# Performance work log

Hardware: AMD Instinct MI355X
Metric: run time of the kernel (lower is better)

The kernel has to match this reference:

```python
import jax, jax.numpy as jnp
import numpy as np

BLOCK = 8
ITERS = 8
EPS = 1e-5
SHAPE = (64, 64, 64)
BATCH = 16


def overlapping_blocks(x, bs):
    # x: [B, M, N, K] -> per-block copies with a 1-cell zero-padded halo:
    # [B, nm, nn, nk, bs+2, bs+2, bs+2]
    B, M, N, K = x.shape
    p = jnp.pad(x, ((0, 0), (1, 1), (1, 1), (1, 1)))

    def gather(a, axis, n, size):
        idx = (jnp.arange(n)[:, None] * bs + jnp.arange(size)[None, :]).reshape(-1)
        a = jnp.take(a, idx, axis=axis)
        return a.reshape(a.shape[:axis] + (n, size) + a.shape[axis + 1:])

    nm, nn, nk = M // bs, N // bs, K // bs
    p = gather(p, 1, nm, bs + 2)   # [B, nm, P, N+2, K+2]
    p = gather(p, 3, nn, bs + 2)   # [B, nm, P, nn, P, K+2]
    p = gather(p, 5, nk, bs + 2)   # [B, nm, P, nn, P, nk, P]
    return p.transpose(0, 1, 3, 5, 2, 4, 6)


def param_blocks(w, bs):
    # [..., M, N, K] -> [..., nm, nn, nk, bs, bs, bs] (non-overlapping)
    lead = w.shape[:-3]
    M, N, K = w.shape[-3:]
    w = w.reshape(*lead, M // bs, bs, N // bs, bs, K // bs, bs)
    nl = len(lead)
    perm = tuple(range(nl)) + (nl, nl + 2, nl + 4, nl + 1, nl + 3, nl + 5)
    return w.transpose(perm)


def gridnet_step(weight, bias, residual_scale, x, inner_iterations, block_size,
                 eps=EPS, normalize=True):
    bs = block_size
    blocks = overlapping_blocks(x, bs)            # [B, nm, nn, nk, P, P, P]
    wb = param_blocks(weight, bs)                 # [27, nm, nn, nk, bs, bs, bs]
    bb = param_blocks(bias, bs)                   # [nm, nn, nk, bs, bs, bs]
    rb = param_blocks(residual_scale, bs)
    inner = (slice(None),) * 4 + (slice(1, -1),) * 3

    for _ in range(inner_iterations):
        if normalize:
            mean = blocks.mean(axis=(-3, -2, -1), keepdims=True)
            var = blocks.var(axis=(-3, -2, -1), keepdims=True)
            normed = (blocks - mean) / jnp.sqrt(var + eps)
        else:
            normed = blocks
        dot = jnp.zeros_like(blocks[inner])
        tap = 0
        for dx in range(3):
            for dy in range(3):
                for dz in range(3):
                    nb = normed[..., dx:dx + bs, dy:dy + bs, dz:dz + bs]
                    dot = dot + nb * wb[tap]
                    tap += 1
        out = blocks[inner] + rb * jax.nn.silu(dot + bb)
        # only interior cells update; halo stays at initial (synced) values
        blocks = blocks.at[inner].set(out)

    y = blocks[inner]                              # [B, nm, nn, nk, bs, bs, bs]
    B, nm, nn, nk = y.shape[:4]
    return y.transpose(0, 1, 4, 2, 5, 3, 6).reshape(B, nm * bs, nn * bs, nk * bs)


def setup_inputs() -> dict:
    key = jax.random.key(0)
    k_w, k_x = jax.random.split(key)
    M, N, K = SHAPE
    weight = jax.random.normal(k_w, (27, M, N, K), dtype=jnp.float32) / np.sqrt(27.0).astype(np.float32)
    bias = jnp.zeros((M, N, K), dtype=jnp.float32)
    residual_scale = jnp.ones((M, N, K), dtype=jnp.float32)
    x = jax.random.normal(k_x, (BATCH, M, N, K), dtype=jnp.float32)
    return {"weight": weight, "bias": bias, "residual_scale": residual_scale, "x": x}


def reference(weight, bias, residual_scale, x):
    return gridnet_step(weight, bias, residual_scale, x, ITERS, BLOCK, EPS, True)
```

## Files before the change

kernel.cpp:

```cpp
#include <hip/hip_runtime.h>

typedef _Float16 h2 __attribute__((ext_vector_type(2)));

#define CSTR 7
#define COLH 14

template <int CTRL>
__device__ __forceinline__ float dpp_stage(float v) {
    int x = __builtin_amdgcn_update_dpp(0, __float_as_int(v), CTRL, 0xf, 0xf, true);
    return v + __int_as_float(x);
}
__device__ __forceinline__ float wave_sum(float v) {
    v = dpp_stage<0x111>(v);
    v = dpp_stage<0x112>(v);
    v = dpp_stage<0x114>(v);
    v = dpp_stage<0x118>(v);
    v = dpp_stage<0x142>(v);
    v = dpp_stage<0x143>(v);
    return v;
}

#define RFL(x) __int_as_float(__builtin_amdgcn_readfirstlane(__float_as_int(x)))

__device__ __forceinline__ h2 mid2(h2 lo, h2 hi) {
    int r = __builtin_amdgcn_alignbit(__builtin_bit_cast(int, hi),
                                      __builtin_bit_cast(int, lo), 16);
    return __builtin_bit_cast(h2, r);
}
__device__ __forceinline__ h2 pkrtz(float a, float b) {
    return __builtin_bit_cast(h2, __builtin_amdgcn_cvt_pkrtz(a, b));
}

#define R27(M) M(0) M(1) M(2) M(3) M(4) M(5) M(6) M(7) M(8) M(9) M(10) M(11) \
    M(12) M(13) M(14) M(15) M(16) M(17) M(18) M(19) M(20) M(21) M(22) M(23)  \
    M(24) M(25) M(26)

#define LOADW(T)                                                               \
    float4 f##T = *(const float4*)(W + ((size_t)(T) << 18) + ofs);             \
    h2 w##T##p = pkrtz(f##T.x, f##T.y);                                        \
    h2 w##T##q = pkrtz(f##T.z, f##T.w);                                        \
    sw0 += f##T.x; sw1 += f##T.y; sw2 += f##T.z; sw3 += f##T.w;

#define COLN(BP, O, T0, T1, T2) {                                              \
    h2 d0 = BP[(O)], d1 = BP[(O) + 1], d2 = BP[(O) + 2];                       \
    h2 m0 = mid2(d0, d1), m1 = mid2(d1, d2);                                   \
    dd0 = __builtin_elementwise_fma(d0, w##T0##p, dd0);                        \
    dd1 = __builtin_elementwise_fma(d1, w##T0##q, dd1);                        \
    dd0 = __builtin_elementwise_fma(m0, w##T1##p, dd0);                        \
    dd1 = __builtin_elementwise_fma(m1, w##T1##q, dd1);                        \
    dd0 = __builtin_elementwise_fma(d1, w##T2##p, dd0);                        \
    dd1 = __builtin_elementwise_fma(d2, w##T2##q, dd1); }

#define SILU(U) ((U) * __builtin_amdgcn_rcpf(1.f + __expf(-(U))))

#define ITERX(BP, DSTB, RED) {                                                 \
    h2 dd0 = { (_Float16)0.f, (_Float16)0.f };                                 \
    h2 dd1 = dd0;                                                              \
    COLN(BP, 0,    0,  1,  2)                                                  \
    COLN(BP, 7,    3,  4,  5)                                                  \
    COLN(BP, 14,   6,  7,  8)                                                  \
    COLN(BP, 70,   9, 10, 11)                                                  \
    COLN(BP, 77,  12, 13, 14)                                                  \
    COLN(BP, 84,  15, 16, 17)                                                  \
    COLN(BP, 140, 18, 19, 20)                                                  \
    COLN(BP, 147, 21, 22, 23)                                                  \
    COLN(BP, 154, 24, 25, 26)                                                  \
    float mean = (halo_s + Si) * inv_n;                                        \
    float istd = rsqrtf((halo_q + Qi) * inv_n - mean * mean + 1e-5f);          \
    float u0 = ((float)dd0.x - mean * sw0) * istd + bf.x;                      \
    float u1 = ((float)dd0.y - mean * sw1) * istd + bf.y;                      \
    float u2 = ((float)dd1.x - mean * sw2) * istd + bf.z;                      \
    float u3 = ((float)dd1.y - mean * sw3) * istd + bf.w;                      \
    c0 += rf.x * SILU(u0);                                                     \
    c1 += rf.y * SILU(u1);                                                     \
    c2 += rf.z * SILU(u2);                                                     \
    c3 += rf.w * SILU(u3);                                                     \
    DSTB[ipc] = (_Float16)c0;                                                  \
    *(h2*)&DSTB[ipc + 1] = pkrtz(c1, c2);                                      \
    DSTB[ipc + 3] = (_Float16)c3;                                              \
    float sp = wave_sum((c0 + c1) + (c2 + c3));                                \
    float qp = wave_sum((c0 * c0 + c1 * c1) + (c2 * c2 + c3 * c3));            \
    if (lane == 63) RED[bh][wv1] = make_float2(sp, qp);                        \
    __syncthreads();                                                           \
    Si = RFL(RED[bh][0].x + RED[bh][1].x);                                     \
    Qi = RFL(RED[bh][0].y + RED[bh][1].y); }

__global__ __launch_bounds__(256)
void gridnet_kernel(const float* __restrict__ W,
                    const float* __restrict__ Bias,
                    const float* __restrict__ Rs,
                    const float* __restrict__ X,
                    float* __restrict__ Y,
                    int n_batch)
{
    __shared__ __align__(16) _Float16 bufA0[100 * COLH];
    __shared__ __align__(16) _Float16 bufA1[100 * COLH];
    __shared__ __align__(16) _Float16 bufB0[100 * COLH];
    __shared__ __align__(16) _Float16 bufB1[100 * COLH];
    __shared__ float4 red4[2][4];
    __shared__ float2 redP[2][2][2];

    const int tid = threadIdx.x;
    const int h    = tid & 1;
    const int ly   = (tid >> 1) & 7;
    const int lx   = (tid >> 4) & 7;
    const int bh   = tid >> 7;
    const int wave = tid >> 6;
    const int lane = tid & 63;
    const int wv1  = wave & 1;

    const int np    = n_batch >> 1;
    const int bid   = blockIdx.x;
    const int r     = bid / np;
    const int pb    = bid - r * np;
    const int batch2 = 2 * pb;
    const int gm0 = (r >> 6) << 3;
    const int gn0 = ((r >> 3) & 7) << 3;
    const int gk0 = (r & 7) << 3;

    const float* xb = X + ((size_t)batch2 << 18);

    float sA_all = 0.f, qA_all = 0.f, sA_int = 0.f, qA_int = 0.f;
    float sB_all = 0.f, qB_all = 0.f, sB_int = 0.f, qB_int = 0.f;
    for (int i = tid; i < 1000; i += 256) {
        int ix = i / 100;
        int rem = i - ix * 100;
        int iy = rem / 10;
        int iz = rem - iy * 10;
        int m = gm0 + ix - 1, n = gn0 + iy - 1, k = gk0 + iz - 1;
        float vA = 0.f, vB = 0.f;
        if ((unsigned)m < 64u && (unsigned)n < 64u && (unsigned)k < 64u) {
            const float* p = xb + (m << 12) + (n << 6) + k;
            vA = p[0];
            vB = p[1 << 18];
        }
        _Float16 hA = (_Float16)vA, hB = (_Float16)vB;
        int a = (ix * 10 + iy) * COLH + iz;
        bufA0[a] = hA; bufA1[a] = hA;
        bufB0[a] = hB; bufB1[a] = hB;
        float fA = (float)hA, fB = (float)hB;
        sA_all += fA; qA_all += fA * fA;
        sB_all += fB; qB_all += fB * fB;
        bool interior = ((unsigned)(ix - 1) < 8u) & ((unsigned)(iy - 1) < 8u) &
                        ((unsigned)(iz - 1) < 8u);
        if (interior) { sA_int += fA; qA_int += fA * fA;
                        sB_int += fB; qB_int += fB * fB; }
    }

    const int gm = gm0 + lx, gn = gn0 + ly;
    const size_t ofs = ((size_t)gm << 12) + (gn << 6) + gk0 + 4 * h;
    float sw0 = 0.f, sw1 = 0.f, sw2 = 0.f, sw3 = 0.f;
    R27(LOADW)
    const float4 bf = *(const float4*)(Bias + ofs);
    const float4 rf = *(const float4*)(Rs + ofs);

    {
        float a0 = wave_sum(sA_all), a1 = wave_sum(qA_all);
        float a2 = wave_sum(sA_int), a3 = wave_sum(qA_int);
        float b0 = wave_sum(sB_all), b1 = wave_sum(qB_all);
        float b2 = wave_sum(sB_int), b3 = wave_sum(qB_int);
        if (lane == 63) {
            red4[0][wave] = make_float4(a0, a1, a2, a3);
            red4[1][wave] = make_float4(b0, b1, b2, b3);
        }
    }
    __syncthreads();

    float S_all = 0.f, Q_all = 0.f, Si = 0.f, Qi = 0.f;
    #pragma unroll
    for (int wv = 0; wv < 4; ++wv) {
        float4 t = red4[bh][wv];
        S_all += t.x; Q_all += t.y; Si += t.z; Qi += t.w;
    }
    const float halo_s = RFL(S_all - Si);
    const float halo_q = RFL(Q_all - Qi);
    Si = RFL(Si); Qi = RFL(Qi);

    _Float16* const my0 = bh ? bufB0 : bufA0;
    _Float16* const my1 = bh ? bufB1 : bufA1;
    const int bpD = (lx * 10 + ly) * CSTR + 2 * h;
    const h2* const bp0 = (const h2*)my0 + bpD;
    const h2* const bp1 = (const h2*)my1 + bpD;
    const int ipc = ((lx + 1) * 10 + (ly + 1)) * COLH + 4 * h + 1;
    float c0 = (float)my0[ipc],     c1 = (float)my0[ipc + 1];
    float c2 = (float)my0[ipc + 2], c3 = (float)my0[ipc + 3];

    const float inv_n = 1.0f / 1000.0f;

    #pragma unroll 1
    for (int it = 0; it < 4; ++it) {
        ITERX(bp0, my1, redP[0])
        ITERX(bp1, my0, redP[1])
    }

    float* yp = Y + ((size_t)(batch2 + bh) << 18) + ofs;
    *(float4*)yp = make_float4(c0, c1, c2, c3);
}

extern "C" void kernel_launch(void* const* d_in, const int* in_sizes, int n_in,
                              void* d_out, int out_size, void* d_ws, size_t ws_size,
                              hipStream_t stream) {
    const float* W = (const float*)d_in[0];
    const float* B = (const float*)d_in[1];
    const float* R = (const float*)d_in[2];
    const float* X = (const float*)d_in[3];
    float* Y = (float*)d_out;

    int n_batch = in_sizes[3] >> 18;
    dim3 grid(512 * (n_batch >> 1)), block(256);
    hipLaunchKernelGGL(gridnet_kernel, grid, block, 0, stream, W, B, R, X, Y, n_batch);
}
```

Before: 167.7 us.

## Process four batch samples per block, two per thread, sharing weight registers

Each block now handles four batch samples instead of two, and each 128-thread half computes two samples per thread. The 27 packed weight taps, bias and residual scale loaded per thread are reused across both samples. This halves the grid size and the weight loads per sample, and merges two samples' reductions into a single barrier per iteration. The cost is doubled LDS usage, more live registers (two sets of accumulators and stats), and fewer blocks to hide latency.

```diff
diff --git a/kernel.cpp b/kernel.cpp
--- a/kernel.cpp
+++ b/kernel.cpp
@@ -41,49 +41,62 @@
     h2 w##T##q = pkrtz(f##T.z, f##T.w);                                        \
     sw0 += f##T.x; sw1 += f##T.y; sw2 += f##T.z; sw3 += f##T.w;
 
-#define COLN(BP, O, T0, T1, T2) {                                              \
+#define COLN(BP, O, T0, T1, T2, D0N, D1N) {                                    \
     h2 d0 = BP[(O)], d1 = BP[(O) + 1], d2 = BP[(O) + 2];                       \
     h2 m0 = mid2(d0, d1), m1 = mid2(d1, d2);                                   \
-    dd0 = __builtin_elementwise_fma(d0, w##T0##p, dd0);                        \
-    dd1 = __builtin_elementwise_fma(d1, w##T0##q, dd1);                        \
-    dd0 = __builtin_elementwise_fma(m0, w##T1##p, dd0);                        \
-    dd1 = __builtin_elementwise_fma(m1, w##T1##q, dd1);                        \
-    dd0 = __builtin_elementwise_fma(d1, w##T2##p, dd0);                        \
-    dd1 = __builtin_elementwise_fma(d2, w##T2##q, dd1); }
+    D0N = __builtin_elementwise_fma(d0, w##T0##p, D0N);                        \
+    D1N = __builtin_elementwise_fma(d1, w##T0##q, D1N);                        \
+    D0N = __builtin_elementwise_fma(m0, w##T1##p, D0N);                        \
+    D1N = __builtin_elementwise_fma(m1, w##T1##q, D1N);                        \
+    D0N = __builtin_elementwise_fma(d1, w##T2##p, D0N);                        \
+    D1N = __builtin_elementwise_fma(d2, w##T2##q, D1N); }
+
+#define DOT27(BP, D0N, D1N)                                                    \
+    COLN(BP, 0,    0,  1,  2, D0N, D1N)                                        \
+    COLN(BP, 7,    3,  4,  5, D0N, D1N)                                        \
+    COLN(BP, 14,   6,  7,  8, D0N, D1N)                                        \
+    COLN(BP, 70,   9, 10, 11, D0N, D1N)                                        \
+    COLN(BP, 77,  12, 13, 14, D0N, D1N)                                        \
+    COLN(BP, 84,  15, 16, 17, D0N, D1N)                                        \
+    COLN(BP, 140, 18, 19, 20, D0N, D1N)                                        \
+    COLN(BP, 147, 21, 22, 23, D0N, D1N)                                        \
+    COLN(BP, 154, 24, 25, 26, D0N, D1N)
 
 #define SILU(U) ((U) * __builtin_amdgcn_rcpf(1.f + __expf(-(U))))
 
-#define ITERX(BP, DSTB, RED) {                                                 \
-    h2 dd0 = { (_Float16)0.f, (_Float16)0.f };                                 \
-    h2 dd1 = dd0;                                                              \
-    COLN(BP, 0,    0,  1,  2)                                                  \
-    COLN(BP, 7,    3,  4,  5)                                                  \
-    COLN(BP, 14,   6,  7,  8)                                                  \
-    COLN(BP, 70,   9, 10, 11)                                                  \
-    COLN(BP, 77,  12, 13, 14)                                                  \
-    COLN(BP, 84,  15, 16, 17)                                                  \
-    COLN(BP, 140, 18, 19, 20)                                                  \
-    COLN(BP, 147, 21, 22, 23)                                                  \
-    COLN(BP, 154, 24, 25, 26)                                                  \
-    float mean = (halo_s + Si) * inv_n;                                        \
-    float istd = rsqrtf((halo_q + Qi) * inv_n - mean * mean + 1e-5f);          \
-    float u0 = ((float)dd0.x - mean * sw0) * istd + bf.x;                      \
-    float u1 = ((float)dd0.y - mean * sw1) * istd + bf.y;                      \
-    float u2 = ((float)dd1.x - mean * sw2) * istd + bf.z;                      \
-    float u3 = ((float)dd1.y - mean * sw3) * istd + bf.w;                      \
-    c0 += rf.x * SILU(u0);                                                     \
-    c1 += rf.y * SILU(u1);                                                     \
-    c2 += rf.z * SILU(u2);                                                     \
-    c3 += rf.w * SILU(u3);                                                     \
-    DSTB[ipc] = (_Float16)c0;                                                  \
-    *(h2*)&DSTB[ipc + 1] = pkrtz(c1, c2);                                      \
-    DSTB[ipc + 3] = (_Float16)c3;                                              \
-    float sp = wave_sum((c0 + c1) + (c2 + c3));                                \
-    float qp = wave_sum((c0 * c0 + c1 * c1) + (c2 * c2 + c3 * c3));            \
-    if (lane == 63) RED[bh][wv1] = make_float2(sp, qp);                        \
+#define EPI4(DD0, DD1, SI, QI, HS, HQ, C0, C1, C2, C3, DSTB) {                 \
+    float mean = (HS + SI) * inv_n;                                            \
+    float istd = rsqrtf((HQ + QI) * inv_n - mean * mean + 1e-5f);              \
+    float u0 = ((float)DD0.x - mean * sw0) * istd + bf.x;                      \
+    float u1 = ((float)DD0.y - mean * sw1) * istd + bf.y;                      \
+    float u2 = ((float)DD1.x - mean * sw2) * istd + bf.z;                      \
+    float u3 = ((float)DD1.y - mean * sw3) * istd + bf.w;                      \
+    C0 += rf.x * SILU(u0);                                                     \
+    C1 += rf.y * SILU(u1);                                                     \
+    C2 += rf.z * SILU(u2);                                                     \
+    C3 += rf.w * SILU(u3);                                                     \
+    DSTB[ipc] = (_Float16)C0;                                                  \
+    *(h2*)&DSTB[ipc + 1] = pkrtz(C1, C2);                                      \
+    DSTB[ipc + 3] = (_Float16)C3;  }
+
+#define ITERP(BPA, DSTA, BPB, DSTB, RED) {                                     \
+    h2 ddA0 = { (_Float16)0.f, (_Float16)0.f };                                \
+    h2 ddA1 = ddA0, ddB0 = ddA0, ddB1 = ddA0;                                  \
+    DOT27(BPA, ddA0, ddA1)                                                     \
+    DOT27(BPB, ddB0, ddB1)                                                     \
+    EPI4(ddA0, ddA1, SiA, QiA, halo_sA, halo_qA, cA0, cA1, cA2, cA3, DSTA)     \
+    EPI4(ddB0, ddB1, SiB, QiB, halo_sB, halo_qB, cB0, cB1, cB2, cB3, DSTB)     \
+    float spA = wave_sum((cA0 + cA1) + (cA2 + cA3));                           \
+    float qpA = wave_sum((cA0 * cA0 + cA1 * cA1) + (cA2 * cA2 + cA3 * cA3));   \
+    float spB = wave_sum((cB0 + cB1) + (cB2 + cB3));                           \
+    float qpB = wave_sum((cB0 * cB0 + cB1 * cB1) + (cB2 * cB2 + cB3 * cB3));   \
+    if (lane == 63) { RED[pg][0][wv1] = make_float2(spA, qpA);                 \
+                      RED[pg][1][wv1] = make_float2(spB, qpB); }               \
     __syncthreads();                                                           \
-    Si = RFL(RED[bh][0].x + RED[bh][1].x);                                     \
-    Qi = RFL(RED[bh][0].y + RED[bh][1].y); }
+    SiA = RFL(RED[pg][0][0].x + RED[pg][0][1].x);                              \
+    QiA = RFL(RED[pg][0][0].y + RED[pg][0][1].y);                              \
+    SiB = RFL(RED[pg][1][0].x + RED[pg][1][1].x);                              \
+    QiB = RFL(RED[pg][1][0].y + RED[pg][1][1].y); }
 
 __global__ __launch_bounds__(256)
 void gridnet_kernel(const float* __restrict__ W,
@@ -93,58 +106,83 @@
                     float* __restrict__ Y,
                     int n_batch)
 {
-    __shared__ __align__(16) _Float16 bufA0[100 * COLH];
-    __shared__ __align__(16) _Float16 bufA1[100 * COLH];
-    __shared__ __align__(16) _Float16 bufB0[100 * COLH];
-    __shared__ __align__(16) _Float16 bufB1[100 * COLH];
-    __shared__ float4 red4[2][4];
-    __shared__ float2 redP[2][2][2];
+    __shared__ __align__(16) _Float16 buf[4][2][100 * COLH];
+    __shared__ float4 red4[4][4];
+    __shared__ float2 redP[2][2][2][2];
 
     const int tid = threadIdx.x;
     const int h    = tid & 1;
     const int ly   = (tid >> 1) & 7;
     const int lx   = (tid >> 4) & 7;
-    const int bh   = tid >> 7;
+    const int pg   = tid >> 7;
     const int wave = tid >> 6;
     const int lane = tid & 63;
     const int wv1  = wave & 1;
 
-    const int np    = n_batch >> 1;
+    const int np    = n_batch >> 2;
     const int bid   = blockIdx.x;
     const int r     = bid / np;
-    const int pb    = bid - r * np;
-    const int batch2 = 2 * pb;
+    const int qb    = bid - r * np;
+    const int batch0 = 4 * qb;
     const int gm0 = (r >> 6) << 3;
     const int gn0 = ((r >> 3) & 7) << 3;
     const int gk0 = (r & 7) << 3;
 
-    const float* xb = X + ((size_t)batch2 << 18);
+    const float* xb = X + ((size_t)batch0 << 18);
 
     float sA_all = 0.f, qA_all = 0.f, sA_int = 0.f, qA_int = 0.f;
     float sB_all = 0.f, qB_all = 0.f, sB_int = 0.f, qB_int = 0.f;
+    float sC_all = 0.f, qC_all = 0.f, sC_int = 0.f, qC_int = 0.f;
+    float sD_all = 0.f, qD_all = 0.f, sD_int = 0.f, qD_int = 0.f;
     for (int i = tid; i < 1000; i += 256) {
         int ix = i / 100;
         int rem = i - ix * 100;
         int iy = rem / 10;
         int iz = rem - iy * 10;
         int m = gm0 + ix - 1, n = gn0 + iy - 1, k = gk0 + iz - 1;
-        float vA = 0.f, vB = 0.f;
+        float vA = 0.f, vB = 0.f, vC = 0.f, vD = 0.f;
         if ((unsigned)m < 64u && (unsigned)n < 64u && (unsigned)k < 64u) {
             const float* p = xb + (m << 12) + (n << 6) + k;
             vA = p[0];
             vB = p[1 << 18];
+            vC = p[2 << 18];
+            vD = p[3 << 18];
         }
         _Float16 hA = (_Float16)vA, hB = (_Float16)vB;
+        _Float16 hC = (_Float16)vC, hD = (_Float16)vD;
         int a = (ix * 10 + iy) * COLH + iz;
-        bufA0[a] = hA; bufA1[a] = hA;
-        bufB0[a] = hB; bufB1[a] = hB;
-        float fA = (float)hA, fB = (float)hB;
+        buf[0][0][a] = hA; buf[0][1][a] = hA;
+        buf[1][0][a] = hB; buf[1][1][a] = hB;
+        buf[2][0][a] = hC; buf[2][1][a] = hC;
+        buf[3][0][a] = hD; buf[3][1][a] = hD;
+        float fA = (float)hA, fB = (float)hB, fC = (float)hC, fD = (float)hD;
         sA_all += fA; qA_all += fA * fA;
         sB_all += fB; qB_all += fB * fB;
+        sC_all += fC; qC_all += fC * fC;
+        sD_all += fD; qD_all += fD * fD;
         bool interior = ((unsigned)(ix - 1) < 8u) & ((unsigned)(iy - 1) < 8u) &
                         ((unsigned)(iz - 1) < 8u);
         if (interior) { sA_int += fA; qA_int += fA * fA;
-                        sB_int += fB; qB_int += fB * fB; }
+                        sB_int += fB; qB_int += fB * fB;
+                        sC_int += fC; qC_int += fC * fC;
+                        sD_int += fD; qD_int += fD * fD; }
+    }
+
+    {
+        float a0 = wave_sum(sA_all), a1 = wave_sum(qA_all);
+        float a2 = wave_sum(sA_int), a3 = wave_sum(qA_int);
+        float b0 = wave_sum(sB_all), b1 = wave_sum(qB_all);
+        float b2 = wave_sum(sB_int), b3 = wave_sum(qB_int);
+        float c0 = wave_sum(sC_all), c1 = wave_sum(qC_all);
+        float c2 = wave_sum(sC_int), c3 = wave_sum(qC_int);
+        float d0 = wave_sum(sD_all), d1 = wave_sum(qD_all);
+        float d2 = wave_sum(sD_int), d3 = wave_sum(qD_int);
+        if (lane == 63) {
+            red4[0][wave] = make_float4(a0, a1, a2, a3);
+            red4[1][wave] = make_float4(b0, b1, b2, b3);
+            red4[2][wave] = make_float4(c0, c1, c2, c3);
+            red4[3][wave] = make_float4(d0, d1, d2, d3);
+        }
     }
 
     const int gm = gm0 + lx, gn = gn0 + ly;
@@ -154,47 +192,48 @@
     const float4 bf = *(const float4*)(Bias + ofs);
     const float4 rf = *(const float4*)(Rs + ofs);
 
-    {
-        float a0 = wave_sum(sA_all), a1 = wave_sum(qA_all);
-        float a2 = wave_sum(sA_int), a3 = wave_sum(qA_int);
-        float b0 = wave_sum(sB_all), b1 = wave_sum(qB_all);
-        float b2 = wave_sum(sB_int), b3 = wave_sum(qB_int);
-        if (lane == 63) {
-            red4[0][wave] = make_float4(a0, a1, a2, a3);
-            red4[1][wave] = make_float4(b0, b1, b2, b3);
-        }
-    }
     __syncthreads();
 
-    float S_all = 0.f, Q_all = 0.f, Si = 0.f, Qi = 0.f;
+    float SA = 0.f, QA = 0.f, SiA = 0.f, QiA = 0.f;
+    float SB = 0.f, QB = 0.f, SiB = 0.f, QiB = 0.f;
     #pragma unroll
     for (int wv = 0; wv < 4; ++wv) {
-        float4 t = red4[bh][wv];
-        S_all += t.x; Q_all += t.y; Si += t.z; Qi += t.w;
-    }
-    const float halo_s = RFL(S_all - Si);
-    const float halo_q = RFL(Q_all - Qi);
-    Si = RFL(Si); Qi = RFL(Qi);
-
-    _Float16* const my0 = bh ? bufB0 : bufA0;
-    _Float16* const my1 = bh ? bufB1 : bufA1;
+        float4 tA = red4[2 * pg][wv];
+        float4 tB = red4[2 * pg + 1][wv];
+        SA += tA.x; QA += tA.y; SiA += tA.z; QiA += tA.w;
+        SB += tB.x; QB += tB.y; SiB += tB.z; QiB += tB.w;
+    }
+    const float halo_sA = RFL(SA - SiA), halo_qA = RFL(QA - QiA);
+    const float halo_sB = RFL(SB - SiB), halo_qB = RFL(QB - QiB);
+    SiA = RFL(SiA); QiA = RFL(QiA);
+    SiB = RFL(SiB); QiB = RFL(QiB);
+
     const int bpD = (lx * 10 + ly) * CSTR + 2 * h;
-    const h2* const bp0 = (const h2*)my0 + bpD;
-    const h2* const bp1 = (const h2*)my1 + bpD;
+    const h2* const bpA0 = (const h2*)buf[2 * pg][0] + bpD;
+    const h2* const bpA1 = (const h2*)buf[2 * pg][1] + bpD;
+    const h2* const bpB0 = (const h2*)buf[2 * pg + 1][0] + bpD;
+    const h2* const bpB1 = (const h2*)buf[2 * pg + 1][1] + bpD;
+    _Float16* const wrA0 = buf[2 * pg][0];
+    _Float16* const wrA1 = buf[2 * pg][1];
+    _Float16* const wrB0 = buf[2 * pg + 1][0];
+    _Float16* const wrB1 = buf[2 * pg + 1][1];
     const int ipc = ((lx + 1) * 10 + (ly + 1)) * COLH + 4 * h + 1;
-    float c0 = (float)my0[ipc],     c1 = (float)my0[ipc + 1];
-    float c2 = (float)my0[ipc + 2], c3 = (float)my0[ipc + 3];
+    float cA0 = (float)wrA0[ipc],     cA1 = (float)wrA0[ipc + 1];
+    float cA2 = (float)wrA0[ipc + 2], cA3 = (float)wrA0[ipc + 3];
+    float cB0 = (float)wrB0[ipc],     cB1 = (float)wrB0[ipc + 1];
+    float cB2 = (float)wrB0[ipc + 2], cB3 = (float)wrB0[ipc + 3];
 
     const float inv_n = 1.0f / 1000.0f;
 
     #pragma unroll 1
     for (int it = 0; it < 4; ++it) {
-        ITERX(bp0, my1, redP[0])
-        ITERX(bp1, my0, redP[1])
-    }
-
-    float* yp = Y + ((size_t)(batch2 + bh) << 18) + ofs;
-    *(float4*)yp = make_float4(c0, c1, c2, c3);
+        ITERP(bpA0, wrA1, bpB0, wrB1, redP[0])
+        ITERP(bpA1, wrA0, bpB1, wrB0, redP[1])
+    }
+
+    float* yp = Y + ((size_t)(batch0 + 2 * pg) << 18) + ofs;
+    *(float4*)yp = make_float4(cA0, cA1, cA2, cA3);
+    *(float4*)(yp + (1 << 18)) = make_float4(cB0, cB1, cB2, cB3);
 }
 
 extern "C" void kernel_launch(void* const* d_in, const int* in_sizes, int n_in,
@@ -207,6 +246,6 @@
     float* Y = (float*)d_out;
 
     int n_batch = in_sizes[3] >> 18;
-    dim3 grid(512 * (n_batch >> 1)), block(256);
+    dim3 grid(512 * (n_batch >> 2)), block(256);
     hipLaunchKernelGGL(gridnet_kernel, grid, block, 0, stream, W, B, R, X, Y, n_batch);
 }
```

New measurement: 155.1 us. -7.5%, faster.
